# Kernel tuning notes

Hardware: AMD Instinct MI355X
Metric: run time of the kernel (lower is better)

Reference implementation:

```python
import jax, jax.numpy as jnp
from jax import lax
import numpy as np

NPOINT = 1024
RADIUS = 0.1
NSAMPLE = 32
BN_EPS = 1e-5


def _fps(xyz, npoint):
    # xyz: [B, N, 3]. Deterministic start at index 0 (torch uses randint seed).
    B, N, _ = xyz.shape

    def step(carry, _):
        dist, far = carry
        centroid = jnp.take_along_axis(xyz, far[:, None, None], axis=1)  # [B,1,3]
        d = jnp.sum((xyz - centroid) ** 2, axis=-1)                      # [B,N]
        dist = jnp.minimum(dist, d)
        nxt = jnp.argmax(dist, axis=-1).astype(jnp.int32)
        return (dist, nxt), far

    init = (jnp.full((B, N), 1e10, xyz.dtype), jnp.zeros((B,), jnp.int32))
    _, idx = lax.scan(step, init, None, length=npoint)
    return jnp.transpose(idx)  # [B, npoint]


def _sqdist(a, b):
    # a: [B,S,3], b: [B,N,3] -> [B,S,N]
    return (jnp.sum(a * a, -1)[:, :, None] + jnp.sum(b * b, -1)[:, None, :]
            - 2.0 * jnp.einsum('bsc,bnc->bsn', a, b))


def _gather(pts, idx):
    # pts: [B,N,C], idx: [B,...] int -> [B,...,C]
    B = pts.shape[0]
    flat = idx.reshape(B, -1)
    out = jnp.take_along_axis(pts, flat[..., None], axis=1)
    return out.reshape(idx.shape + (pts.shape[-1],))


def _ball_query(radius, nsample, xyz, new_xyz):
    B, N, _ = xyz.shape
    sq = _sqdist(new_xyz, xyz)                                        # [B,S,N]
    ar = jnp.arange(N, dtype=jnp.int32)[None, None, :]
    gi = jnp.where(sq > radius ** 2, N, ar)                           # out-of-ball -> N
    gi = jnp.sort(gi, axis=-1)[:, :, :nsample]                        # [B,S,K]
    first = gi[:, :, :1]
    return jnp.where(gi == N, first, gi)                              # pad with first


def _sa_forward(xyz, points, params):
    # torch layout in: xyz [B,3,N], points [B,D,N]
    xyz = jnp.transpose(xyz, (0, 2, 1))        # [B,N,3]
    points = jnp.transpose(points, (0, 2, 1))  # [B,N,D]
    fps_idx = lax.stop_gradient(_fps(xyz, NPOINT))          # [B,S]
    new_xyz = _gather(xyz, fps_idx)                          # [B,S,3]
    idx = _ball_query(RADIUS, NSAMPLE, xyz, new_xyz)         # [B,S,K]
    g_xyz = _gather(xyz, idx) - new_xyz[:, :, None, :]       # [B,S,K,3]
    g_pts = _gather(points, idx)                             # [B,S,K,D]
    x = jnp.concatenate([g_xyz, g_pts], axis=-1)             # [B,S,K,3+D]
    for (W, b, g, bt, m, v) in params:
        x = jnp.einsum('bskc,oc->bsko', x, W) + b            # 1x1 conv
        x = (x - m) * (g / jnp.sqrt(v + BN_EPS)) + bt        # eval-mode BN
        x = jax.nn.relu(x)
    feat = jnp.max(x, axis=2)                                # max over K -> [B,S,C']
    return jnp.transpose(feat, (0, 2, 1))                    # [B,C',S]


def setup_inputs() -> dict:
    key = jax.random.key(0)
    ks = jax.random.split(key, 16)
    B, N = 4, 8192
    d = {}
    d['xyz'] = jax.random.uniform(ks[0], (B, 3, N), jnp.float32)       # unit cube cloud
    d['points'] = jax.random.normal(ks[1], (B, 3, N), jnp.float32)     # e.g. normals
    dims = [(6, 64), (64, 64), (64, 128)]
    k = 2
    for li, (cin, cout) in enumerate(dims, start=1):
        d[f'w{li}'] = jax.random.normal(ks[k], (cout, cin), jnp.float32) * (1.0 / np.sqrt(cin)); k += 1
        d[f'b{li}'] = jnp.zeros((cout,), jnp.float32)
        d[f'g{li}'] = jnp.ones((cout,), jnp.float32)
        d[f't{li}'] = jnp.zeros((cout,), jnp.float32)
        d[f'm{li}'] = jax.random.normal(ks[k], (cout,), jnp.float32) * 0.01; k += 1
        d[f'v{li}'] = jnp.ones((cout,), jnp.float32)
    return d


def reference(xyz, points,
              w1, b1, g1, t1, m1, v1,
              w2, b2, g2, t2, m2, v2,
              w3, b3, g3, t3, m3, v3):
    params = [(w1, b1, g1, t1, m1, v1),
              (w2, b2, g2, t2, m2, v2),
              (w3, b3, g3, t3, m3, v3)]
    return _sa_forward(xyz, points, params)
```

## Files before the change

### kernel.cpp

```cpp
#include <hip/hip_runtime.h>
#include <math.h>

#define NPTS 8192
#define NPOINT 1024
#define NSAMPLE 32

template <int CTRL>
__device__ __forceinline__ unsigned long long dpp_umax64(unsigned long long key) {
  int lo = (int)(unsigned)key;
  int hi = (int)(unsigned)(key >> 32);
  int slo = __builtin_amdgcn_update_dpp(0, lo, CTRL, 0xF, 0xF, true);
  int shi = __builtin_amdgcn_update_dpp(0, hi, CTRL, 0xF, 0xF, true);
  unsigned long long o =
      ((unsigned long long)(unsigned)shi << 32) | (unsigned)slo;
  return (o > key) ? o : key;
}

__global__ __launch_bounds__(256, 1) void fps_kernel(
    const float* __restrict__ xyz, const float2* __restrict__ sxy_g,
    const float* __restrict__ sz_g, const unsigned* __restrict__ io_g32,
    const float* __restrict__ anch_g, float* __restrict__ new_xyz) {
#pragma clang fp contract(off)
  extern __shared__ char smem[];
  float2* xyL = (float2*)smem;
  float2* zdL = (float2*)(smem + 65536);
  unsigned* ioL32 = (unsigned*)(smem + 131072);
  const unsigned short* ioL16 = (const unsigned short*)(smem + 131072);
  unsigned long long* ck = (unsigned long long*)(smem + 147456);
  unsigned long long* red = (unsigned long long*)(smem + 149504);

  const int b = blockIdx.x;
  const int t = threadIdx.x;
  const int w = t >> 6, l = t & 63;
  const int myCell = l * 4 + ((w + l) & 3);

  const float2* sxy = sxy_g + (size_t)b * NPTS;
  const float* sz = sz_g + (size_t)b * NPTS;
#pragma unroll
  for (int m = 0; m < 32; ++m) {
    int i = m * 256 + t;
    xyL[i] = sxy[i];
    zdL[i] = make_float2(sz[i], 1e10f);
  }
  const unsigned* iog = io_g32 + (size_t)b * 4096;
#pragma unroll
  for (int m = 0; m < 16; ++m) { int i = m * 256 + t; ioL32[i] = iog[i]; }

  const float* ag = anch_g + ((size_t)b * 256 + myCell) * 6;
  const float ax = ag[0], ay = ag[1], az = ag[2];
  const float hx = ag[3], hy = ag[4], hz = ag[5];
  float ckv = __uint_as_float(0x7F800000u);

  const float* xp0 = xyz + (size_t)b * 3 * NPTS;
  float cx = xp0[0], cy = xp0[NPTS], cz = xp0[2 * NPTS];
  float* outp = new_xyz + (size_t)b * NPOINT * 3;
  if (t == 0) { outp[0] = cx; outp[1] = cy; outp[2] = cz; }
  __syncthreads();

  const int half = l >> 5, li = l & 31;
  for (int s = 1; s < NPOINT; ++s) {
    float tx = fmaxf(fabsf(cx - ax) - hx, 0.f);
    float ty = fmaxf(fabsf(cy - ay) - hy, 0.f);
    float tz = fmaxf(fabsf(cz - az) - hz, 0.f);
    float L = (tx * tx + ty * ty) + tz * tz;
    bool active = !(L * 0.9999f >= ckv);
    unsigned long long mask = __ballot(active);
    while (mask) {
      int c0 = (int)(__ffsll((long long)mask) - 1);
      mask &= mask - 1;
      int c1 = c0;
      if (mask) { c1 = (int)(__ffsll((long long)mask) - 1); mask &= mask - 1; }
      int cl = half ? c1 : c0;
      int cellC = cl * 4 + ((w + cl) & 3);
      int pt = cellC * 32 + li;
      float2 xy = xyL[pt];
      float2 zd = zdL[pt];
      float dx = xy.x - cx;
      float dy = xy.y - cy;
      float dz = zd.x - cz;
      float d = (dx * dx + dy * dy) + dz * dz;
      float dm = fminf(zd.y, d);
      ((float*)&zdL[pt])[1] = dm;
      unsigned orig = (unsigned)ioL16[pt];
      unsigned long long kk =
          ((unsigned long long)__float_as_uint(dm) << 26) |
          ((unsigned long long)(8191u - orig) << 13) | (unsigned)pt;
      kk = dpp_umax64<0x111>(kk);
      kk = dpp_umax64<0x112>(kk);
      kk = dpp_umax64<0x114>(kk);
      kk = dpp_umax64<0x118>(kk);
      kk = dpp_umax64<0x142>(kk);
      if (l == 31 || l == 63) ck[cellC] = kk;
    }
    unsigned long long kl = ck[myCell];
    ckv = __uint_as_float((unsigned)(kl >> 26));
    unsigned long long kr = kl;
    kr = dpp_umax64<0x111>(kr);
    kr = dpp_umax64<0x112>(kr);
    kr = dpp_umax64<0x114>(kr);
    kr = dpp_umax64<0x118>(kr);
    kr = dpp_umax64<0x142>(kr);
    kr = dpp_umax64<0x143>(kr);
    if (l == 63) red[(s & 1) * 4 + w] = kr;
    __syncthreads();
    const unsigned long long* rp = red + (s & 1) * 4;
    unsigned long long k0 = rp[0], k1 = rp[1], k2 = rp[2], k3 = rp[3];
    unsigned long long ka = (k0 > k1) ? k0 : k1;
    unsigned long long kb = (k2 > k3) ? k2 : k3;
    unsigned long long km = (ka > kb) ? ka : kb;
    unsigned ptw = (unsigned)(km & 8191ull);
    float2 xyw = xyL[ptw];
    float zw = zdL[ptw].x;
    cx = xyw.x; cy = xyw.y; cz = zw;
    if (t == 0) { outp[3 * s] = cx; outp[3 * s + 1] = cy; outp[3 * s + 2] = cz; }
  }
}

__global__ __launch_bounds__(256, 1) void setup_kernel(
    const float* __restrict__ xyz, const float* __restrict__ w3,
    const float* __restrict__ b1, const float* __restrict__ g1, const float* __restrict__ t1,
    const float* __restrict__ m1, const float* __restrict__ v1,
    const float* __restrict__ b2, const float* __restrict__ g2, const float* __restrict__ t2,
    const float* __restrict__ m2, const float* __restrict__ v2,
    const float* __restrict__ b3, const float* __restrict__ g3, const float* __restrict__ t3,
    const float* __restrict__ m3, const float* __restrict__ v3,
    float2* __restrict__ sxy_g, float* __restrict__ sz_g,
    unsigned short* __restrict__ io_g, float* __restrict__ anch_g,
    float* __restrict__ w3t, float* __restrict__ scsh) {
#pragma clang fp contract(off)
  __shared__ unsigned cnt[256];
  __shared__ unsigned scan[256];
  const int b = blockIdx.x;
  const int t = threadIdx.x;
  const float* xp = xyz + (size_t)b * 3 * NPTS;
  cnt[t] = 0;
  __syncthreads();
  float xr[32], yr[32], zr[32];
  int cr[32];
#pragma unroll
  for (int m = 0; m < 32; ++m) {
    int i = m * 256 + t;
    float x = xp[i], y = xp[NPTS + i], z = xp[2 * NPTS + i];
    int xi = max(0, min((int)(x * 8.f), 7));
    int yi = max(0, min((int)(y * 8.f), 7));
    int zi = max(0, min((int)(z * 4.f), 3));
    int c = (zi << 6) | (yi << 3) | xi;
    xr[m] = x; yr[m] = y; zr[m] = z; cr[m] = c;
    atomicAdd(&cnt[c], 1u);
  }
  __syncthreads();
  unsigned v = cnt[t];
  scan[t] = v;
  __syncthreads();
  for (int off = 1; off < 256; off <<= 1) {
    unsigned u = (t >= off) ? scan[t - off] : 0u;
    __syncthreads();
    scan[t] += u;
    __syncthreads();
  }
  cnt[t] = scan[t] - v;
  __syncthreads();
#pragma unroll
  for (int m = 0; m < 32; ++m) {
    unsigned p = atomicAdd(&cnt[cr[m]], 1u);
    sxy_g[(size_t)b * NPTS + p] = make_float2(xr[m], yr[m]);
    sz_g[(size_t)b * NPTS + p] = zr[m];
    io_g[(size_t)b * NPTS + p] = (unsigned short)(m * 256 + t);
  }
  __syncthreads();
  {
    float mnx = 1e30f, mny = 1e30f, mnz = 1e30f;
    float mxx = -1e30f, mxy = -1e30f, mxz = -1e30f;
    for (int e = 0; e < 32; ++e) {
      float2 xy = sxy_g[(size_t)b * NPTS + t * 32 + e];
      float z = sz_g[(size_t)b * NPTS + t * 32 + e];
      mnx = fminf(mnx, xy.x); mxx = fmaxf(mxx, xy.x);
      mny = fminf(mny, xy.y); mxy = fmaxf(mxy, xy.y);
      mnz = fminf(mnz, z);    mxz = fmaxf(mxz, z);
    }
    float cax = 0.5f * (mnx + mxx), cay = 0.5f * (mny + mxy), caz = 0.5f * (mnz + mxz);
    float* agp = anch_g + ((size_t)b * 256 + t) * 6;
    agp[0] = cax; agp[1] = cay; agp[2] = caz;
    agp[3] = fmaxf(mxx - cax, cax - mnx) * 1.000002f;
    agp[4] = fmaxf(mxy - cay, cay - mny) * 1.000002f;
    agp[5] = fmaxf(mxz - caz, caz - mnz) * 1.000002f;
  }
  if (b != 0) return;
  for (int i = t; i < 8192; i += 256) {
    int o = i >> 6, c = i & 63;
    w3t[c * 128 + o] = w3[i];
  }
  if (t < 64) {
    float s = g1[t] / sqrtf(v1[t] + 1e-5f);
    scsh[t] = s;
    scsh[64 + t] = (b1[t] - m1[t]) * s + t1[t];
    float s2 = g2[t] / sqrtf(v2[t] + 1e-5f);
    scsh[128 + t] = s2;
    scsh[192 + t] = (b2[t] - m2[t]) * s2 + t2[t];
  }
  if (t < 128) {
    float s3 = g3[t] / sqrtf(v3[t] + 1e-5f);
    scsh[256 + t] = s3;
    scsh[384 + t] = (b3[t] - m3[t]) * s3 + t3[t];
  }
}

__global__ __launch_bounds__(256, 2) void mlp_kernel(
    const float* __restrict__ xyz, const float* __restrict__ points,
    const float* __restrict__ new_xyz,
    const float* __restrict__ w1, const float* __restrict__ w2,
    const float* __restrict__ w3t, const float* __restrict__ scsh,
    float* __restrict__ out) {
  __shared__ float act[256 * 64];
  float4* act4 = (float4*)act;
  const int tid = threadIdx.x;
  const int wv = tid >> 6, lane = tid & 63;
  const int s0 = blockIdx.x * 8;
  const int b = s0 >> 10;
  const int g = tid >> 5;
  const int k = tid & 31;
  const int gc = s0 + g;
  const float* xp = xyz + (size_t)b * 3 * NPTS;
  const float* pp = points + (size_t)b * 3 * NPTS;

  int* slots = (int*)(act + wv * 4096);
  {
#pragma clang fp contract(off)
    for (int h = 0; h < 2; ++h) {
      const int hc = s0 + 2 * wv + h;
      const float* cp0 = new_xyz + (size_t)hc * 3;
      const float cx = cp0[0], cy = cp0[1], cz = cp0[2];
      const float asq = (cx * cx + cy * cy) + cz * cz;
      int cnt = 0;
      for (int base = 0; base < NPTS; base += 64) {
        int n = base + lane;
        float x = xp[n], y = xp[NPTS + n], z = xp[2 * NPTS + n];
        float bsq = (x * x + y * y) + z * z;
        float ab = (x * cx + y * cy) + z * cz;
        float sq = (asq + bsq) - 2.0f * ab;
        bool inc = !(sq > 0.01f);
        unsigned long long mk = __ballot(inc);
        int pos = cnt + (int)__popcll(mk & ((1ull << lane) - 1ull));
        if (inc && pos < NSAMPLE) slots[h * 32 + pos] = n;
        cnt += (int)__popcll(mk);
        if (cnt >= NSAMPLE) break;
      }
      if (lane < NSAMPLE) {
        int first = slots[h * 32];
        int v = (lane < cnt) ? slots[h * 32 + lane] : first;
        slots[h * 32 + lane] = v;
      }
    }
  }
  const int n = slots[(g & 1) * 32 + k];

  const float* cp = new_xyz + (size_t)gc * 3;
  float f0 = xp[n] - cp[0];
  float f1 = xp[NPTS + n] - cp[1];
  float f2 = xp[2 * NPTS + n] - cp[2];
  float f3 = pp[n];
  float f4 = pp[NPTS + n];
  float f5 = pp[2 * NPTS + n];
  const float* sc1 = scsh;        const float* sh1 = scsh + 64;
  const float* sc2 = scsh + 128;  const float* sh2 = scsh + 192;
  const float* sc3 = scsh + 256;  const float* sh3 = scsh + 384;
  const int row = tid;

#pragma unroll
  for (int oc = 0; oc < 16; ++oc) {
    float va[4];
#pragma unroll
    for (int jj = 0; jj < 4; ++jj) {
      int o = oc * 4 + jj;
      const float* wr = w1 + o * 6;
      float a = f0 * wr[0] + f1 * wr[1] + f2 * wr[2] +
                f3 * wr[3] + f4 * wr[4] + f5 * wr[5];
      va[jj] = fmaxf(a * sc1[o] + sh1[o], 0.f);
    }
    act4[row * 16 + (oc ^ (row & 15))] = make_float4(va[0], va[1], va[2], va[3]);
  }

  float acc[64];
#pragma unroll
  for (int o = 0; o < 64; ++o) acc[o] = 0.f;
  for (int cc = 0; cc < 16; ++cc) {
    float4 av = act4[row * 16 + (cc ^ (row & 15))];
#pragma unroll
    for (int o = 0; o < 64; ++o) {
      const float* wr = w2 + o * 64 + cc * 4;
      acc[o] += av.x * wr[0] + av.y * wr[1] + av.z * wr[2] + av.w * wr[3];
    }
  }
#pragma unroll
  for (int oc = 0; oc < 16; ++oc) {
    float va[4];
#pragma unroll
    for (int jj = 0; jj < 4; ++jj) {
      int o = oc * 4 + jj;
      va[jj] = fmaxf(acc[o] * sc2[o] + sh2[o], 0.f);
    }
    act4[row * 16 + (oc ^ (row & 15))] = make_float4(va[0], va[1], va[2], va[3]);
  }
  __syncthreads();

  const int j = k;
  const int sb = gc & 1023;
  for (int ph = 0; ph < 2; ++ph) {
    int o3a = ph * 64 + j;
    int o3b = o3a + 32;
    float wa[64], wb[64];
#pragma unroll
    for (int c = 0; c < 64; ++c) {
      wa[c] = w3t[c * 128 + o3a];
      wb[c] = w3t[c * 128 + o3b];
    }
    float sca = sc3[o3a], sha = sh3[o3a];
    float scb = sc3[o3b], shb = sh3[o3b];
    float vma = 0.f, vmb = 0.f;
    for (int kk = 0; kk < 32; ++kk) {
      int r2 = g * 32 + kk;
      float a0 = 0.f, a1 = 0.f, a2 = 0.f, a3 = 0.f;
      float b0 = 0.f, b1 = 0.f, b2 = 0.f, b3 = 0.f;
#pragma unroll
      for (int cc = 0; cc < 16; cc += 4) {
        float4 u0 = act4[r2 * 16 + ((cc + 0) ^ (r2 & 15))];
        float4 u1 = act4[r2 * 16 + ((cc + 1) ^ (r2 & 15))];
        float4 u2 = act4[r2 * 16 + ((cc + 2) ^ (r2 & 15))];
        float4 u3 = act4[r2 * 16 + ((cc + 3) ^ (r2 & 15))];
        a0 += u0.x * wa[4*cc+0]  + u0.y * wa[4*cc+1]  + u0.z * wa[4*cc+2]  + u0.w * wa[4*cc+3];
        a1 += u1.x * wa[4*cc+4]  + u1.y * wa[4*cc+5]  + u1.z * wa[4*cc+6]  + u1.w * wa[4*cc+7];
        a2 += u2.x * wa[4*cc+8]  + u2.y * wa[4*cc+9]  + u2.z * wa[4*cc+10] + u2.w * wa[4*cc+11];
        a3 += u3.x * wa[4*cc+12] + u3.y * wa[4*cc+13] + u3.z * wa[4*cc+14] + u3.w * wa[4*cc+15];
        b0 += u0.x * wb[4*cc+0]  + u0.y * wb[4*cc+1]  + u0.z * wb[4*cc+2]  + u0.w * wb[4*cc+3];
        b1 += u1.x * wb[4*cc+4]  + u1.y * wb[4*cc+5]  + u1.z * wb[4*cc+6]  + u1.w * wb[4*cc+7];
        b2 += u2.x * wb[4*cc+8]  + u2.y * wb[4*cc+9]  + u2.z * wb[4*cc+10] + u2.w * wb[4*cc+11];
        b3 += u3.x * wb[4*cc+12] + u3.y * wb[4*cc+13] + u3.z * wb[4*cc+14] + u3.w * wb[4*cc+15];
      }
      float xa = (a0 + a1) + (a2 + a3);
      float xb = (b0 + b1) + (b2 + b3);
      vma = fmaxf(vma, fmaxf(xa * sca + sha, 0.f));
      vmb = fmaxf(vmb, fmaxf(xb * scb + shb, 0.f));
    }
    out[((size_t)b * 128 + o3a) * 1024 + sb] = vma;
    out[((size_t)b * 128 + o3b) * 1024 + sb] = vmb;
  }
}

extern "C" void kernel_launch(void* const* d_in, const int* in_sizes, int n_in,
                              void* d_out, int out_size, void* d_ws, size_t ws_size,
                              hipStream_t stream) {
  (void)in_sizes; (void)n_in; (void)out_size; (void)ws_size;
  const float* xyz    = (const float*)d_in[0];
  const float* points = (const float*)d_in[1];
  const float* w1 = (const float*)d_in[2];
  const float* b1 = (const float*)d_in[3];
  const float* g1 = (const float*)d_in[4];
  const float* t1 = (const float*)d_in[5];
  const float* m1 = (const float*)d_in[6];
  const float* v1 = (const float*)d_in[7];
  const float* w2 = (const float*)d_in[8];
  const float* b2 = (const float*)d_in[9];
  const float* g2 = (const float*)d_in[10];
  const float* t2 = (const float*)d_in[11];
  const float* m2 = (const float*)d_in[12];
  const float* v2 = (const float*)d_in[13];
  const float* w3 = (const float*)d_in[14];
  const float* b3 = (const float*)d_in[15];
  const float* g3 = (const float*)d_in[16];
  const float* t3 = (const float*)d_in[17];
  const float* m3 = (const float*)d_in[18];
  const float* v3 = (const float*)d_in[19];

  float* wsf = (float*)d_ws;
  float* new_xyz = wsf;
  float* w3t     = wsf + 12288;
  float* scsh    = wsf + 20480;
  float2* sxy_g  = (float2*)(wsf + 20992);
  float* sz_g    = wsf + 86528;
  unsigned short* io_g = (unsigned short*)(wsf + 119296);
  float* anch_g  = wsf + 135680;
  float* out     = (float*)d_out;

  hipFuncSetAttribute(reinterpret_cast<const void*>(fps_kernel),
                      hipFuncAttributeMaxDynamicSharedMemorySize, 149568);

  hipLaunchKernelGGL(setup_kernel, dim3(4), dim3(256), 0, stream,
                     xyz, w3, b1, g1, t1, m1, v1, b2, g2, t2, m2, v2,
                     b3, g3, t3, m3, v3, sxy_g, sz_g, io_g, anch_g, w3t, scsh);
  hipLaunchKernelGGL(fps_kernel, dim3(4), dim3(256), 149568, stream,
                     xyz, sxy_g, sz_g, (const unsigned*)io_g, anch_g, new_xyz);
  hipLaunchKernelGGL(mlp_kernel, dim3(512), dim3(256), 0, stream,
                     xyz, points, new_xyz, w1, w2, w3t, scsh, out);
}
```

Measured before the change: 1.457 ms.

## Process active FPS cells four lanes per cell with per-thread 8-point reduction

The FPS inner loop now compacts the active cells into a per-wave shared list and assigns four lanes per cell, with each lane handling 8 points. Previously two cells were processed per wave iteration at 32 lanes each. Each lane does a register-level max tree before a two-step DPP reduction. Shared arrays get a 33-stride padding to avoid bank conflicts on the strided 8-point loads, and the 8191-orig key term is precomputed in setup. The intent is to handle 16 cells per round and shorten the DPP chains. The cost is more registers and extra shared memory.

```diff
diff --git a/kernel.cpp b/kernel.cpp
--- a/kernel.cpp
+++ b/kernel.cpp
@@ -18,16 +18,17 @@
 
 __global__ __launch_bounds__(256, 1) void fps_kernel(
     const float* __restrict__ xyz, const float2* __restrict__ sxy_g,
-    const float* __restrict__ sz_g, const unsigned* __restrict__ io_g32,
+    const float* __restrict__ sz_g, const unsigned* __restrict__ ko_g32,
     const float* __restrict__ anch_g, float* __restrict__ new_xyz) {
 #pragma clang fp contract(off)
   extern __shared__ char smem[];
   float2* xyL = (float2*)smem;
-  float2* zdL = (float2*)(smem + 65536);
-  unsigned* ioL32 = (unsigned*)(smem + 131072);
-  const unsigned short* ioL16 = (const unsigned short*)(smem + 131072);
-  unsigned long long* ck = (unsigned long long*)(smem + 147456);
-  unsigned long long* red = (unsigned long long*)(smem + 149504);
+  float2* zdL = (float2*)(smem + 67584);
+  unsigned* koL32 = (unsigned*)(smem + 135168);
+  const unsigned short* koL16 = (const unsigned short*)(smem + 135168);
+  unsigned long long* ck = (unsigned long long*)(smem + 151552);
+  unsigned long long* red = (unsigned long long*)(smem + 153600);
+  unsigned* alist = (unsigned*)(smem + 153664);
 
   const int b = blockIdx.x;
   const int t = threadIdx.x;
@@ -39,12 +40,13 @@
 #pragma unroll
   for (int m = 0; m < 32; ++m) {
     int i = m * 256 + t;
-    xyL[i] = sxy[i];
-    zdL[i] = make_float2(sz[i], 1e10f);
-  }
-  const unsigned* iog = io_g32 + (size_t)b * 4096;
-#pragma unroll
-  for (int m = 0; m < 16; ++m) { int i = m * 256 + t; ioL32[i] = iog[i]; }
+    int phys = (i >> 5) * 33 + (i & 31);
+    xyL[phys] = sxy[i];
+    zdL[phys] = make_float2(sz[i], 1e10f);
+  }
+  const unsigned* kog = ko_g32 + (size_t)b * 4096;
+#pragma unroll
+  for (int m = 0; m < 16; ++m) { int i = m * 256 + t; koL32[i] = kog[i]; }
 
   const float* ag = anch_g + ((size_t)b * 256 + myCell) * 6;
   const float ax = ag[0], ay = ag[1], az = ag[2];
@@ -57,7 +59,8 @@
   if (t == 0) { outp[0] = cx; outp[1] = cy; outp[2] = cz; }
   __syncthreads();
 
-  const int half = l >> 5, li = l & 31;
+  unsigned* alw = alist + w * 64;
+  const int q = l >> 2, ql = l & 3;
   for (int s = 1; s < NPOINT; ++s) {
     float tx = fmaxf(fabsf(cx - ax) - hx, 0.f);
     float ty = fmaxf(fabsf(cy - ay) - hy, 0.f);
@@ -65,32 +68,46 @@
     float L = (tx * tx + ty * ty) + tz * tz;
     bool active = !(L * 0.9999f >= ckv);
     unsigned long long mask = __ballot(active);
-    while (mask) {
-      int c0 = (int)(__ffsll((long long)mask) - 1);
-      mask &= mask - 1;
-      int c1 = c0;
-      if (mask) { c1 = (int)(__ffsll((long long)mask) - 1); mask &= mask - 1; }
-      int cl = half ? c1 : c0;
-      int cellC = cl * 4 + ((w + cl) & 3);
-      int pt = cellC * 32 + li;
-      float2 xy = xyL[pt];
-      float2 zd = zdL[pt];
-      float dx = xy.x - cx;
-      float dy = xy.y - cy;
-      float dz = zd.x - cz;
-      float d = (dx * dx + dy * dy) + dz * dz;
-      float dm = fminf(zd.y, d);
-      ((float*)&zdL[pt])[1] = dm;
-      unsigned orig = (unsigned)ioL16[pt];
-      unsigned long long kk =
-          ((unsigned long long)__float_as_uint(dm) << 26) |
-          ((unsigned long long)(8191u - orig) << 13) | (unsigned)pt;
-      kk = dpp_umax64<0x111>(kk);
-      kk = dpp_umax64<0x112>(kk);
-      kk = dpp_umax64<0x114>(kk);
-      kk = dpp_umax64<0x118>(kk);
-      kk = dpp_umax64<0x142>(kk);
-      if (l == 31 || l == 63) ck[cellC] = kk;
+    int A = (int)__popcll(mask);
+    if (active) {
+      int rank = (int)__popcll(mask & ((1ull << l) - 1ull));
+      alw[rank] = (unsigned)myCell;
+    }
+    const int rounds = (A + 15) >> 4;
+    for (int r = 0; r < rounds; ++r) {
+      int idx = r * 16 + q;
+      if (idx >= A) idx = A - 1;
+      int cellC = (int)alw[idx];
+      int pb = ql * 8;
+      int phys = cellC * 33 + pb;
+      int lpt = cellC * 32 + pb;
+      uint4 k4 = *((const uint4*)(koL16 + lpt));
+      float2 xyv[8], zdv[8];
+#pragma unroll
+      for (int e = 0; e < 8; ++e) { xyv[e] = xyL[phys + e]; zdv[e] = zdL[phys + e]; }
+      unsigned kos[8] = {k4.x & 0xFFFFu, k4.x >> 16, k4.y & 0xFFFFu, k4.y >> 16,
+                         k4.z & 0xFFFFu, k4.z >> 16, k4.w & 0xFFFFu, k4.w >> 16};
+      unsigned long long keys[8];
+#pragma unroll
+      for (int e = 0; e < 8; ++e) {
+        float dx = xyv[e].x - cx;
+        float dy = xyv[e].y - cy;
+        float dz = zdv[e].x - cz;
+        float d = (dx * dx + dy * dy) + dz * dz;
+        float dm = fminf(zdv[e].y, d);
+        ((float*)&zdL[phys + e])[1] = dm;
+        keys[e] = ((unsigned long long)__float_as_uint(dm) << 26) |
+                  ((unsigned long long)kos[e] << 13) | (unsigned)(lpt + e);
+      }
+#pragma unroll
+      for (int st = 1; st < 8; st <<= 1)
+#pragma unroll
+        for (int e = 0; e < 8; e += 2 * st)
+          keys[e] = (keys[e + st] > keys[e]) ? keys[e + st] : keys[e];
+      unsigned long long tk = keys[0];
+      tk = dpp_umax64<0xB1>(tk);
+      tk = dpp_umax64<0x4E>(tk);
+      if (ql == 3) ck[cellC] = tk;
     }
     unsigned long long kl = ck[myCell];
     ckv = __uint_as_float((unsigned)(kl >> 26));
@@ -109,8 +126,9 @@
     unsigned long long kb = (k2 > k3) ? k2 : k3;
     unsigned long long km = (ka > kb) ? ka : kb;
     unsigned ptw = (unsigned)(km & 8191ull);
-    float2 xyw = xyL[ptw];
-    float zw = zdL[ptw].x;
+    int pphys = (int)(ptw >> 5) * 33 + (int)(ptw & 31u);
+    float2 xyw = xyL[pphys];
+    float zw = zdL[pphys].x;
     cx = xyw.x; cy = xyw.y; cz = zw;
     if (t == 0) { outp[3 * s] = cx; outp[3 * s + 1] = cy; outp[3 * s + 2] = cz; }
   }
@@ -125,7 +143,7 @@
     const float* __restrict__ b3, const float* __restrict__ g3, const float* __restrict__ t3,
     const float* __restrict__ m3, const float* __restrict__ v3,
     float2* __restrict__ sxy_g, float* __restrict__ sz_g,
-    unsigned short* __restrict__ io_g, float* __restrict__ anch_g,
+    unsigned short* __restrict__ ko_g, float* __restrict__ anch_g,
     float* __restrict__ w3t, float* __restrict__ scsh) {
 #pragma clang fp contract(off)
   __shared__ unsigned cnt[256];
@@ -165,7 +183,7 @@
     unsigned p = atomicAdd(&cnt[cr[m]], 1u);
     sxy_g[(size_t)b * NPTS + p] = make_float2(xr[m], yr[m]);
     sz_g[(size_t)b * NPTS + p] = zr[m];
-    io_g[(size_t)b * NPTS + p] = (unsigned short)(m * 256 + t);
+    ko_g[(size_t)b * NPTS + p] = (unsigned short)(8191 - (m * 256 + t));
   }
   __syncthreads();
   {
@@ -377,18 +395,18 @@
   float* scsh    = wsf + 20480;
   float2* sxy_g  = (float2*)(wsf + 20992);
   float* sz_g    = wsf + 86528;
-  unsigned short* io_g = (unsigned short*)(wsf + 119296);
+  unsigned short* ko_g = (unsigned short*)(wsf + 119296);
   float* anch_g  = wsf + 135680;
   float* out     = (float*)d_out;
 
   hipFuncSetAttribute(reinterpret_cast<const void*>(fps_kernel),
-                      hipFuncAttributeMaxDynamicSharedMemorySize, 149568);
+                      hipFuncAttributeMaxDynamicSharedMemorySize, 154688);
 
   hipLaunchKernelGGL(setup_kernel, dim3(4), dim3(256), 0, stream,
                      xyz, w3, b1, g1, t1, m1, v1, b2, g2, t2, m2, v2,
-                     b3, g3, t3, m3, v3, sxy_g, sz_g, io_g, anch_g, w3t, scsh);
-  hipLaunchKernelGGL(fps_kernel, dim3(4), dim3(256), 149568, stream,
-                     xyz, sxy_g, sz_g, (const unsigned*)io_g, anch_g, new_xyz);
+                     b3, g3, t3, m3, v3, sxy_g, sz_g, ko_g, anch_g, w3t, scsh);
+  hipLaunchKernelGGL(fps_kernel, dim3(4), dim3(256), 154688, stream,
+                     xyz, sxy_g, sz_g, (const unsigned*)ko_g, anch_g, new_xyz);
   hipLaunchKernelGGL(mlp_kernel, dim3(512), dim3(256), 0, stream,
                      xyz, points, new_xyz, w1, w2, w3t, scsh, out);
 }
```

Measured after the change: 1.427 ms. 2.1% less time.
